# Kernel optimization log

Hardware: AMD Instinct MI355X
Metric: run time of the kernel (lower is better)

The kernel has to match this reference:

```python
import jax, jax.numpy as jnp
import numpy as np

B, T, D = 16, 4096, 1024


def setup_inputs() -> dict:
    key = jax.random.key(0)
    kx, kl = jax.random.split(key)
    x = jax.random.normal(kx, (B, T, D), dtype=jnp.float32)
    seq_lens = jax.random.randint(kl, (B,), 0, T + 1, dtype=jnp.int64)
    return {"x": x, "seq_lens": seq_lens}


def reference(x, seq_lens):
    # mask[i, :length] = True over [B, T] (broadcast over D), then flatten + compact.
    # Torch's flatten()[mask.flatten()] is row-major, so within each valid (b, t)
    # the D features stay contiguous -> gather whole rows of x.reshape(B*T, D).
    b, t, d = x.shape
    valid = jnp.arange(t)[None, :] < seq_lens[:, None]          # [B, T] bool
    total_rows = int(np.asarray(seq_lens).sum())                # static under eager eval
    rows = jnp.nonzero(valid.ravel(), size=total_rows, fill_value=0)[0]  # [total_rows]
    return x.reshape(b * t, d)[rows].reshape(-1)                # [total_rows * D]
```

## Files before the change

kernel.cpp:

```cpp
#include <hip/hip_runtime.h>


#define DD 1024
#define TT 4096

__global__ void prefix_kernel(const void* __restrict__ seq_raw, int n,
                              int total_rows, int* __restrict__ prefix) {
    if (blockIdx.x == 0 && threadIdx.x == 0) {
        const int*       s32 = (const int*)seq_raw;
        const long long* s64 = (const long long*)seq_raw;
        long long sum32 = 0;
        for (int i = 0; i < n; ++i) sum32 += (long long)s32[i];
        const bool use32 = (sum32 == (long long)total_rows);
        int acc = 0;
        for (int i = 0; i < n; ++i) {
            prefix[i] = acc;
            acc += use32 ? s32[i] : (int)s64[i];
        }
        prefix[n] = acc;
    }
}

__global__ __launch_bounds__(256) void gather_rows(
        const float* __restrict__ x, const int* __restrict__ prefix,
        float* __restrict__ out, int n_b) {
    const int r = blockIdx.x;
    int b = 0;
    for (int i = 1; i <= n_b; ++i) b += (prefix[i] <= r) ? 1 : 0;
    const int t = r - prefix[b];
    const float4* __restrict__ src =
        (const float4*)(x + ((size_t)b * TT + (size_t)t) * DD);
    float4* __restrict__ dst = (float4*)(out + (size_t)r * DD);
    dst[threadIdx.x] = src[threadIdx.x];
}

extern "C" void kernel_launch(void* const* d_in, const int* in_sizes, int n_in,
                              void* d_out, int out_size, void* d_ws, size_t ws_size,
                              hipStream_t stream) {
    const float* x   = (const float*)d_in[0];
    const void*  seq = d_in[1];
    const int    n_b = in_sizes[1];
    float*       out = (float*)d_out;
    int*      prefix = (int*)d_ws;

    const int total_rows = out_size / DD;

    prefix_kernel<<<1, 64, 0, stream>>>(seq, n_b, total_rows, prefix);
    if (total_rows > 0) {
        gather_rows<<<total_rows, 256, 0, stream>>>(x, prefix, out, n_b);
    }
}
```

Baseline: 342.1 us.

## Fuse prefix computation into gather kernel with grid-stride float4 copy

Drops the separate single-thread prefix kernel. Every block now recomputes the 16-entry prefix of seq_lens in registers, which removes one launch and the serialized dependency between the two kernels. The gather becomes a grid-stride loop over float4 elements with the grid capped at 2048 blocks. In exchange, every thread repeats the batch lookup per element, and the batch count is hardcoded to 16.

```diff
diff --git a/kernel.cpp b/kernel.cpp
--- a/kernel.cpp
+++ b/kernel.cpp
@@ -3,50 +3,52 @@
 
 #define DD 1024
 #define TT 4096
-
-__global__ void prefix_kernel(const void* __restrict__ seq_raw, int n,
-                              int total_rows, int* __restrict__ prefix) {
-    if (blockIdx.x == 0 && threadIdx.x == 0) {
-        const int*       s32 = (const int*)seq_raw;
-        const long long* s64 = (const long long*)seq_raw;
-        long long sum32 = 0;
-        for (int i = 0; i < n; ++i) sum32 += (long long)s32[i];
-        const bool use32 = (sum32 == (long long)total_rows);
-        int acc = 0;
-        for (int i = 0; i < n; ++i) {
-            prefix[i] = acc;
-            acc += use32 ? s32[i] : (int)s64[i];
-        }
-        prefix[n] = acc;
-    }
-}
+#define NB 16
 
 __global__ __launch_bounds__(256) void gather_rows(
-        const float* __restrict__ x, const int* __restrict__ prefix,
-        float* __restrict__ out, int n_b) {
-    const int r = blockIdx.x;
-    int b = 0;
-    for (int i = 1; i <= n_b; ++i) b += (prefix[i] <= r) ? 1 : 0;
-    const int t = r - prefix[b];
-    const float4* __restrict__ src =
-        (const float4*)(x + ((size_t)b * TT + (size_t)t) * DD);
-    float4* __restrict__ dst = (float4*)(out + (size_t)r * DD);
-    dst[threadIdx.x] = src[threadIdx.x];
+        const float4* __restrict__ x, const void* __restrict__ seq_raw,
+        float4* __restrict__ out, int total_rows) {
+    const int*       s32 = (const int*)seq_raw;
+    const long long* s64 = (const long long*)seq_raw;
+    long long sum32 = 0;
+#pragma unroll
+    for (int i = 0; i < NB; ++i) sum32 += (long long)s32[i];
+    const bool use32 = (sum32 == (long long)total_rows);
+
+    int pfx[NB + 1];
+    pfx[0] = 0;
+#pragma unroll
+    for (int i = 0; i < NB; ++i)
+        pfx[i + 1] = pfx[i] + (use32 ? s32[i] : (int)s64[i]);
+
+    const int n4     = total_rows << 8;
+    const int stride = gridDim.x * blockDim.x;
+    for (int j = blockIdx.x * blockDim.x + threadIdx.x; j < n4; j += stride) {
+        const int r = j >> 8;
+        int b = 0, base = 0;
+#pragma unroll
+        for (int i = 1; i <= NB; ++i) {
+            const bool c = (pfx[i] <= r);
+            b   += c;
+            base = c ? pfx[i] : base;
+        }
+        const int t = r - base;
+        out[j] = x[(((size_t)b * TT + (size_t)t) << 8) + (size_t)(j & 255)];
+    }
 }
 
 extern "C" void kernel_launch(void* const* d_in, const int* in_sizes, int n_in,
                               void* d_out, int out_size, void* d_ws, size_t ws_size,
                               hipStream_t stream) {
-    const float* x   = (const float*)d_in[0];
-    const void*  seq = d_in[1];
-    const int    n_b = in_sizes[1];
-    float*       out = (float*)d_out;
-    int*      prefix = (int*)d_ws;
+    const float4* x   = (const float4*)d_in[0];
+    const void*   seq = d_in[1];
+    float4*       out = (float4*)d_out;
 
     const int total_rows = out_size / DD;
+    if (total_rows <= 0) return;
 
-    prefix_kernel<<<1, 64, 0, stream>>>(seq, n_b, total_rows, prefix);
-    if (total_rows > 0) {
-        gather_rows<<<total_rows, 256, 0, stream>>>(x, prefix, out, n_b);
-    }
+    const int n4     = total_rows << 8;
+    int       blocks = (n4 + 255) / 256;
+    if (blocks > 2048) blocks = 2048;
+    gather_rows<<<blocks, 256, 0, stream>>>(x, seq, out, total_rows);
 }
```

New measurement: 349.5 us. 1.02x slower.
